# Kernel optimization log

Hardware: AMD Instinct MI355X
Metric: run time of the kernel (lower is better)

Reference implementation:

```python
import math
import jax, jax.numpy as jnp
import numpy as np

H, W = 24, 24
N = H * W
D = 1024
B = 32
MAX_ITERS = 6

# 9 relative neighbor offsets (3x3 window, row-major)
_REL = np.array([[-1, -1], [-1, 0], [-1, 1], [0, -1], [0, 0], [0, 1], [1, -1], [1, 0], [1, 1]])


def _neighbor_cols():
    y, x = np.meshgrid(np.arange(H), np.arange(W), indexing='ij')
    ny = np.clip(y[None] + _REL[:, 0, None, None], 0, H - 1)  # [9,H,W]
    nx = np.clip(x[None] + _REL[:, 1, None, None], 0, W - 1)
    return jnp.asarray((ny * W + nx).reshape(9, N))  # [9,N]


def setup_inputs() -> dict:
    key = jax.random.key(0)
    ks = jax.random.split(key, 8)
    return {
        'tok2d': jax.random.normal(ks[0], (B, N + 1, D), dtype=jnp.float32),
        'dw_w': jax.random.normal(ks[1], (D, 1, 3, 3), dtype=jnp.float32) * 0.02,
        'pw_w': jax.random.normal(ks[2], (9, D, 1, 1), dtype=jnp.float32) * 0.02,
        'pw_b': jnp.zeros((9,), dtype=jnp.float32),
        'q_w': jax.random.normal(ks[3], (D, D), dtype=jnp.float32) * 0.02,
        'q_b': jax.random.normal(ks[4], (D,), dtype=jnp.float32) * 0.02,
        'v_w': jax.random.normal(ks[5], (D, D), dtype=jnp.float32) * 0.02,
        'v_b': jax.random.normal(ks[6], (D,), dtype=jnp.float32) * 0.02,
        'K': 256,
        'MAX_TOKENS': 128,
    }


def _affinity_head(patch2d, dw_w, pw_w, pw_b):
    # patch2d: [B,H,W,D] -> Q: [B,H,W,9]
    x = jnp.transpose(patch2d, (0, 3, 1, 2))  # NCHW
    x = jax.lax.conv_general_dilated(
        x, dw_w, window_strides=(1, 1), padding='SAME',
        feature_group_count=D,
        dimension_numbers=('NCHW', 'OIHW', 'NCHW'))
    x = jnp.einsum('bdhw,od->bohw', x, pw_w[:, :, 0, 0]) + pw_b[None, :, None, None]
    return jax.nn.softmax(jnp.transpose(x, (0, 2, 3, 1)), axis=-1)


def _build_token_affinity(Q):
    # Q: [B,H,W,9] -> A: [B,N,N] via 9 shifted-neighbor scatters
    cols = _neighbor_cols()                                   # [9,N]
    rows = jnp.broadcast_to(jnp.arange(N)[None, :], (9, N))   # [9,N]
    vals = jnp.moveaxis(Q.reshape(-1, N, 9), -1, 1).reshape(-1, 9 * N)  # [B,9*N]
    A = jnp.zeros((Q.shape[0], N, N), dtype=Q.dtype)
    return A.at[:, rows.reshape(-1), cols.reshape(-1)].add(vals)


def _cluster_roots(A):
    roots = jnp.argmax(A, axis=-1)  # [B,N]
    for _ in range(MAX_ITERS):      # pointer jumping (idempotent once converged)
        roots = jnp.take_along_axis(roots, roots, axis=1)
    return roots


def _cluster_centers(E, roots, K):
    b = E.shape[0]
    bidx = jnp.arange(b)[:, None]
    centers_sum = jnp.zeros_like(E).at[bidx, roots].add(E)          # [B,N,D]
    counts = jnp.zeros(E.shape[:2], E.dtype).at[bidx, roots].add(1.0)  # [B,N]
    _, topk_idx = jax.lax.top_k(counts, K)
    ord_idx = jnp.sort(topk_idx, axis=1)
    cs = jnp.take_along_axis(centers_sum, ord_idx[:, :, None], axis=1)
    cnt = jnp.take_along_axis(counts, ord_idx, axis=1)
    C = cs / jnp.clip(cnt, 1.0, None)[:, :, None]
    return C, cnt


def reference(tok2d, dw_w, pw_w, pw_b, q_w, q_b, v_w, v_b, K, MAX_TOKENS):
    cls_tok = tok2d[:, :1, :]                 # [B,1,D]
    patch = tok2d[:, 1:, :]                   # [B,N,D]
    Q = _affinity_head(patch.reshape(-1, H, W, D), dw_w, pw_w, pw_b)
    A = _build_token_affinity(Q)
    roots = _cluster_roots(A)
    C, cnt = _cluster_centers(patch, roots, K)
    Q_cls = cls_tok @ q_w.T + q_b             # [B,1,D]
    K_v = C @ v_w.T + v_b                     # [B,K,D]
    scores = jnp.einsum('bod,bkd->bk', Q_cls, K_v) / math.sqrt(D)
    valid = jnp.where(cnt > 0, scores, -jnp.inf)
    m = min(MAX_TOKENS, C.shape[1])
    _, idx = jax.lax.top_k(valid, m)
    idx_sorted = jnp.sort(idx, axis=-1)
    return jnp.take_along_axis(C, idx_sorted[:, :, None], axis=1)  # [B,m,D]
```

## Files before the change

kernel.cpp:

```cpp
#include <hip/hip_runtime.h>
#include <math.h>

#define Hh 24
#define Ww 24
#define Nn 576
#define Dd 1024
#define Bb 32
#define Kk 256
#define Mm 128
#define TOKSTRIDE (577 * 1024)

#define R0_OFF 0
#define MEMB_OFF 1152
#define OFFS_OFF 1728
#define ORD_OFF 2304
#define CNT_OFF 2560
#define P_OFF 2944
#define QC_OFF 3776
#define U_OFF 4800
#define T_OFF 5824
#define UP_OFF 6144

__device__ __forceinline__ float* batch_base(float* out, int b) {
  return out + (size_t)b * Mm * Dd;
}

__device__ __forceinline__ float wave_sum_dpp(float x) {
  int y;
  y = __builtin_amdgcn_update_dpp(0, __float_as_int(x), 0x111, 0xf, 0xf, true);
  x += __int_as_float(y);
  y = __builtin_amdgcn_update_dpp(0, __float_as_int(x), 0x112, 0xf, 0xf, true);
  x += __int_as_float(y);
  y = __builtin_amdgcn_update_dpp(0, __float_as_int(x), 0x114, 0xf, 0xf, true);
  x += __int_as_float(y);
  y = __builtin_amdgcn_update_dpp(0, __float_as_int(x), 0x118, 0xf, 0xf, true);
  x += __int_as_float(y);
  y = __builtin_amdgcn_update_dpp(0, __float_as_int(x), 0x142, 0xa, 0xf, true);
  x += __int_as_float(y);
  y = __builtin_amdgcn_update_dpp(0, __float_as_int(x), 0x143, 0xc, 0xf, true);
  x += __int_as_float(y);
  return x;
}

__global__ __launch_bounds__(256) void qcls_kernel(
    const float* __restrict__ tok2d, const float* __restrict__ q_w,
    const float* __restrict__ q_b, float* __restrict__ outb) {
  int dp = blockIdx.x;
  int wave = threadIdx.x >> 6;
  int lane = threadIdx.x & 63;
  float4 qv[4];
#pragma unroll
  for (int i = 0; i < 4; i++)
    qv[i] = *(const float4*)(q_w + (size_t)dp * Dd + lane * 4 + 256 * i);
  float qb = q_b[dp];
  for (int bb = 0; bb < 8; bb++) {
    int b = wave * 8 + bb;
    const float* cls = tok2d + (size_t)b * TOKSTRIDE;
    float a = 0.f;
#pragma unroll
    for (int i = 0; i < 4; i++) {
      float4 cv = *(const float4*)(cls + lane * 4 + 256 * i);
      a += qv[i].x * cv.x + qv[i].y * cv.y + qv[i].z * cv.z + qv[i].w * cv.w;
    }
    a = wave_sum_dpp(a);
    if (lane == 63) batch_base(outb, b)[QC_OFF + dp] = a + qb;
  }
}

__global__ __launch_bounds__(256) void u_part_kernel(const float* __restrict__ v_w,
                                                     float* __restrict__ outb) {
  int b = blockIdx.x >> 3;
  int chunk = blockIdx.x & 7;
  int tid = threadIdx.x;
  int d0 = tid * 4;
  float* basef = batch_base(outb, b);
  __shared__ float qs[128];
  if (tid < 128) qs[tid] = basef[QC_OFF + chunk * 128 + tid];
  __syncthreads();
  float4 a = make_float4(0.f, 0.f, 0.f, 0.f);
#pragma unroll 4
  for (int dpl = 0; dpl < 128; dpl++) {
    int dp = chunk * 128 + dpl;
    float4 vv = *(const float4*)(v_w + (size_t)dp * Dd + d0);
    float qq = qs[dpl];
    a.x += qq * vv.x; a.y += qq * vv.y; a.z += qq * vv.z; a.w += qq * vv.w;
  }
  *(float4*)(basef + UP_OFF + chunk * Dd + d0) = a;
}

__global__ __launch_bounds__(256) void combine_ut_kernel(
    const float* __restrict__ v_b, float* __restrict__ outb) {
  int b = blockIdx.x;
  int tid = threadIdx.x;
  float* basef = batch_base(outb, b);
  int d0 = tid * 4;
  float4 s = make_float4(0.f, 0.f, 0.f, 0.f);
#pragma unroll
  for (int c = 0; c < 8; c++) {
    float4 v = *(const float4*)(basef + UP_OFF + c * Dd + d0);
    s.x += v.x; s.y += v.y; s.z += v.z; s.w += v.w;
  }
  *(float4*)(basef + U_OFF + d0) = s;

  float a = 0.f;
  for (int i = tid; i < Dd; i += 256) a += basef[QC_OFF + i] * v_b[i];
  __shared__ float sh[256];
  sh[tid] = a;
  __syncthreads();
  for (int st = 128; st > 0; st >>= 1) {
    if (tid < st) sh[tid] += sh[tid + st];
    __syncthreads();
  }
  if (tid == 0) basef[T_OFF] = sh[0];
}

__global__ __launch_bounds__(256, 3) void affinity_p_root_kernel(
    const float* __restrict__ tok2d, const float* __restrict__ dw_w,
    const float* __restrict__ pw_w, const float* __restrict__ pw_b,
    float* __restrict__ outb) {
  int wave = threadIdx.x >> 6;
  int lane = threadIdx.x & 63;
  int blk = (blockIdx.x & 7) * (Bb * Hh * 3 / 8) + (blockIdx.x >> 3);
  int b = blk / (Hh * 3);
  int rem = blk % (Hh * 3);
  int y = rem / 3;
  int x0 = (rem % 3) * 8;
  int d0 = wave * 256 + lane * 4;
  const float* patch = tok2d + (size_t)b * TOKSTRIDE + Dd;
  float* basef = batch_base(outb, b);

  union { float4 v[9]; float f[36]; } w;
  const float4* dwp = (const float4*)(dw_w + (size_t)d0 * 9);
#pragma unroll
  for (int j = 0; j < 9; j++) w.v[j] = dwp[j];
  float4 pw[9];
#pragma unroll
  for (int o = 0; o < 9; o++)
    pw[o] = *(const float4*)(pw_w + (size_t)o * Dd + d0);
  float4 u4 = *(const float4*)(basef + U_OFF + d0);

  __shared__ float red[8][4][10];

  float4 cc[8];
  float pacc[8];
#pragma unroll
  for (int t = 0; t < 8; t++) {
    cc[t] = make_float4(0.f, 0.f, 0.f, 0.f);
    pacc[t] = 0.f;
  }
#pragma unroll
  for (int ky = 0; ky < 3; ky++) {
    int yy = y + ky - 1;
    if (yy < 0 || yy >= Hh) continue;
    const float* prow = patch + (size_t)(yy * Ww) * Dd + d0;
    float4 wA = make_float4(0.f, 0.f, 0.f, 0.f);
    if (x0 > 0) wA = *(const float4*)(prow + (size_t)(x0 - 1) * Dd);
    float4 wB = *(const float4*)(prow + (size_t)x0 * Dd);
    int kA = ky * 3, kB = ky * 3 + 1, kC = ky * 3 + 2;
#pragma unroll
    for (int t = 0; t < 8; t++) {
      float4 wC = make_float4(0.f, 0.f, 0.f, 0.f);
      int xx = x0 + t + 1;
      if (xx < Ww) wC = *(const float4*)(prow + (size_t)xx * Dd);
      cc[t].x += wA.x * w.f[kA] + wB.x * w.f[kB] + wC.x * w.f[kC];
      cc[t].y += wA.y * w.f[9 + kA] + wB.y * w.f[9 + kB] + wC.y * w.f[9 + kC];
      cc[t].z += wA.z * w.f[18 + kA] + wB.z * w.f[18 + kB] + wC.z * w.f[18 + kC];
      cc[t].w += wA.w * w.f[27 + kA] + wB.w * w.f[27 + kB] + wC.w * w.f[27 + kC];
      if (ky == 1)
        pacc[t] = wB.x * u4.x + wB.y * u4.y + wB.z * u4.z + wB.w * u4.w;
      wA = wB;
      wB = wC;
    }
  }

#pragma unroll
  for (int t = 0; t < 8; t++) {
    float acc[10];
#pragma unroll
    for (int o = 0; o < 9; o++) {
      acc[o] = cc[t].x * pw[o].x + cc[t].y * pw[o].y + cc[t].z * pw[o].z +
               cc[t].w * pw[o].w;
    }
    acc[9] = pacc[t];
#pragma unroll
    for (int o = 0; o < 10; o++) acc[o] = wave_sum_dpp(acc[o]);
    if (lane == 63) {
#pragma unroll
      for (int o = 0; o < 10; o++) red[t][wave][o] = acc[o];
    }
  }
  __syncthreads();

  if (threadIdx.x < 8) {
    int t = threadIdx.x;
    int x = x0 + t;
    int n = y * Ww + x;
    float l[9], q[9];
    float mx = -INFINITY;
#pragma unroll
    for (int o = 0; o < 9; o++) {
      l[o] = red[t][0][o] + red[t][1][o] + red[t][2][o] + red[t][3][o] + pw_b[o];
      mx = fmaxf(mx, l[o]);
    }
    float ssum = 0.f;
#pragma unroll
    for (int o = 0; o < 9; o++) {
      q[o] = expf(l[o] - mx);
      ssum += q[o];
    }
#pragma unroll
    for (int o = 0; o < 9; o++) q[o] = q[o] / ssum;

    int cols[9];
    float vals[9];
    int ncol = 0;
    for (int o = 0; o < 9; o++) {
      int dy = o / 3 - 1, dx = o % 3 - 1;
      int ny = min(max(y + dy, 0), Hh - 1);
      int nx = min(max(x + dx, 0), Ww - 1);
      int col = ny * Ww + nx;
      int f = -1;
      for (int j = 0; j < ncol; j++)
        if (cols[j] == col) { f = j; break; }
      if (f >= 0) vals[f] += q[o];
      else { cols[ncol] = col; vals[ncol] = q[o]; ncol++; }
    }
    float best = -1.f;
    int bcol = 1 << 30;
    for (int j = 0; j < ncol; j++) {
      if (vals[j] > best || (vals[j] == best && cols[j] < bcol)) {
        best = vals[j];
        bcol = cols[j];
      }
    }
    ((int*)basef)[R0_OFF + n] = bcol;
    basef[P_OFF + n] = red[t][0][9] + red[t][1][9] + red[t][2][9] + red[t][3][9];
  }
}

__global__ __launch_bounds__(576) void cluster_topk_kernel(float* __restrict__ outb) {
  int b = blockIdx.x;
  int n = threadIdx.x;
  int* base = (int*)batch_base(outb, b);
  __shared__ int ra[Nn], rb[Nn], scnt[Nn], soff[Nn];
  ra[n] = base[R0_OFF + n];
  scnt[n] = 0;
  __syncthreads();
  for (int it = 0; it < 6; it++) {
    rb[n] = ra[ra[n]];
    __syncthreads();
    ra[n] = rb[n];
    __syncthreads();
  }
  int r = ra[n];
  atomicAdd(&scnt[r], 1);
  __syncthreads();

  soff[n] = scnt[n];
  __syncthreads();
  for (int s = 1; s < Nn; s <<= 1) {
    int v = (n >= s) ? soff[n - s] : 0;
    __syncthreads();
    soff[n] += v;
    __syncthreads();
  }
  int excl = soff[n] - scnt[n];
  base[OFFS_OFF + n] = excl;
  int offr = soff[r] - scnt[r];
  int rk = 0;
  for (int m = 0; m < n; m++) rk += (ra[m] == r);
  base[MEMB_OFF + offr + rk] = n;

  int cn = scnt[n];
  int rank = 0;
  for (int m = 0; m < Nn; m++) {
    int cm = scnt[m];
    rank += (cm > cn) || (cm == cn && m < n);
  }
  int sl = (rank < Kk) ? 1 : 0;
  rb[n] = sl;
  __syncthreads();
  for (int s = 1; s < Nn; s <<= 1) {
    int v = (n >= s) ? rb[n - s] : 0;
    __syncthreads();
    rb[n] += v;
    __syncthreads();
  }
  if (sl) {
    int pos = rb[n] - 1;
    base[ORD_OFF + pos] = n;
    base[CNT_OFF + pos] = cn;
  }
}

__global__ __launch_bounds__(256) void scores_plan_kernel(float* __restrict__ outb) {
  int b = blockIdx.x;
  int tid = threadIdx.x;
  int wave = tid >> 6, lane = tid & 63;
  float* basef = batch_base(outb, b);
  int* base = (int*)basef;
  __shared__ int s_mem[Nn], s_off[Nn], s_ord[Kk], s_cnt[Kk], s_out[Mm];
  __shared__ float ss[Kk];
  __shared__ int sel[Kk];
  for (int i = tid; i < Nn; i += 256) {
    s_mem[i] = base[MEMB_OFF + i];
    s_off[i] = base[OFFS_OFF + i];
  }
  s_ord[tid] = base[ORD_OFF + tid];
  s_cnt[tid] = base[CNT_OFF + tid];
  float tt = basef[T_OFF];
  __syncthreads();

  int idx = s_ord[tid];
  int c = s_cnt[tid];
  float s;
  if (c > 0) {
    int off = s_off[idx];
    float sum = 0.f;
    for (int j = 0; j < c; j++) sum += basef[P_OFF + s_mem[off + j]];
    s = (sum / (float)c + tt) * (1.0f / 32.0f);
  } else {
    s = -INFINITY;
  }
  ss[tid] = s;
  __syncthreads();

  float vk = ss[tid];
  int rank = 0;
  for (int m = 0; m < Kk; m++) {
    float vm = ss[m];
    rank += (vm > vk) || (vm == vk && m < tid);
  }
  sel[tid] = (rank < Mm) ? 1 : 0;
  __syncthreads();
  if (sel[tid]) {
    int pos = 0;
    for (int m = 0; m < tid; m++) pos += sel[m];
    s_out[pos] = tid;
  }
  __syncthreads();

  for (int kp = wave; kp < Mm; kp += 4) {
    int k = s_out[kp];
    int kidx = s_ord[k];
    int kc = s_cnt[k];
    int koff = s_off[kidx];
    int* row = base + kp * Dd;
    if (lane == 0) row[0] = kc;
    for (int j = lane; j < kc; j += 64) row[1 + j] = s_mem[koff + j];
  }
}

__global__ __launch_bounds__(256) void output_kernel(
    const float* __restrict__ tok2d, float* __restrict__ outb) {
  int blk = blockIdx.x;
  int b = blk / Mm;
  int tid = threadIdx.x;
  float* rowf = outb + (size_t)blk * Dd;
  int* rowi = (int*)rowf;
  __shared__ int s_c;
  __shared__ int s_m[Nn];
  if (tid == 0) s_c = rowi[0];
  __syncthreads();
  int c = s_c;
  for (int j = tid; j < c; j += 256) s_m[j] = rowi[1 + j];
  __syncthreads();
  const float* patch = tok2d + (size_t)b * TOKSTRIDE + Dd;
  int d0 = tid * 4;
  float4 acc = make_float4(0.f, 0.f, 0.f, 0.f);
  for (int j = 0; j < c; j++) {
    float4 rv = *(const float4*)(patch + (size_t)s_m[j] * Dd + d0);
    acc.x += rv.x; acc.y += rv.y; acc.z += rv.z; acc.w += rv.w;
  }
  float inv = 1.0f / (float)max(c, 1);
  *(float4*)(rowf + d0) =
      make_float4(acc.x * inv, acc.y * inv, acc.z * inv, acc.w * inv);
}

extern "C" void kernel_launch(void* const* d_in, const int* in_sizes, int n_in,
                              void* d_out, int out_size, void* d_ws,
                              size_t ws_size, hipStream_t stream) {
  const float* tok2d = (const float*)d_in[0];
  const float* dw_w = (const float*)d_in[1];
  const float* pw_w = (const float*)d_in[2];
  const float* pw_b = (const float*)d_in[3];
  const float* q_w = (const float*)d_in[4];
  const float* q_b = (const float*)d_in[5];
  const float* v_w = (const float*)d_in[6];
  const float* v_b = (const float*)d_in[7];
  float* out = (float*)d_out;
  (void)d_ws; (void)ws_size;

  qcls_kernel<<<dim3(Dd), dim3(256), 0, stream>>>(tok2d, q_w, q_b, out);
  u_part_kernel<<<dim3(Bb * 8), dim3(256), 0, stream>>>(v_w, out);
  combine_ut_kernel<<<dim3(Bb), dim3(256), 0, stream>>>(v_b, out);
  affinity_p_root_kernel<<<dim3(Bb * Hh * 3), dim3(256), 0, stream>>>(
      tok2d, dw_w, pw_w, pw_b, out);
  cluster_topk_kernel<<<dim3(Bb), dim3(Nn), 0, stream>>>(out);
  scores_plan_kernel<<<dim3(Bb), dim3(256), 0, stream>>>(out);
  output_kernel<<<dim3(Bb * Mm), dim3(256), 0, stream>>>(tok2d, out);
}
```

Before: 249.7 us.

## Raise affinity kernel occupancy, defer pw loads, shorten DPP reduction, unroll root selection

```diff
diff --git a/kernel.cpp b/kernel.cpp
--- a/kernel.cpp
+++ b/kernel.cpp
@@ -42,6 +42,19 @@
   return x;
 }
 
+__device__ __forceinline__ float row_sum_dpp(float x) {
+  int y;
+  y = __builtin_amdgcn_update_dpp(0, __float_as_int(x), 0x111, 0xf, 0xf, true);
+  x += __int_as_float(y);
+  y = __builtin_amdgcn_update_dpp(0, __float_as_int(x), 0x112, 0xf, 0xf, true);
+  x += __int_as_float(y);
+  y = __builtin_amdgcn_update_dpp(0, __float_as_int(x), 0x114, 0xf, 0xf, true);
+  x += __int_as_float(y);
+  y = __builtin_amdgcn_update_dpp(0, __float_as_int(x), 0x118, 0xf, 0xf, true);
+  x += __int_as_float(y);
+  return x;
+}
+
 __global__ __launch_bounds__(256) void qcls_kernel(
     const float* __restrict__ tok2d, const float* __restrict__ q_w,
     const float* __restrict__ q_b, float* __restrict__ outb) {
@@ -114,7 +127,7 @@
   if (tid == 0) basef[T_OFF] = sh[0];
 }
 
-__global__ __launch_bounds__(256, 3) void affinity_p_root_kernel(
+__global__ __launch_bounds__(256, 4) void affinity_p_root_kernel(
     const float* __restrict__ tok2d, const float* __restrict__ dw_w,
     const float* __restrict__ pw_w, const float* __restrict__ pw_b,
     float* __restrict__ outb) {
@@ -129,17 +142,13 @@
   const float* patch = tok2d + (size_t)b * TOKSTRIDE + Dd;
   float* basef = batch_base(outb, b);
 
+  __shared__ float red[8 * 167 + 8];
+
   union { float4 v[9]; float f[36]; } w;
   const float4* dwp = (const float4*)(dw_w + (size_t)d0 * 9);
 #pragma unroll
   for (int j = 0; j < 9; j++) w.v[j] = dwp[j];
-  float4 pw[9];
-#pragma unroll
-  for (int o = 0; o < 9; o++)
-    pw[o] = *(const float4*)(pw_w + (size_t)o * Dd + d0);
   float4 u4 = *(const float4*)(basef + U_OFF + d0);
-
-  __shared__ float red[8][4][10];
 
   float4 cc[8];
   float pacc[8];
@@ -173,6 +182,13 @@
     }
   }
 
+  __builtin_amdgcn_sched_barrier(0);
+
+  float4 pw[9];
+#pragma unroll
+  for (int o = 0; o < 9; o++)
+    pw[o] = *(const float4*)(pw_w + (size_t)o * Dd + d0);
+
 #pragma unroll
   for (int t = 0; t < 8; t++) {
     float acc[10];
@@ -183,23 +199,31 @@
     }
     acc[9] = pacc[t];
 #pragma unroll
-    for (int o = 0; o < 10; o++) acc[o] = wave_sum_dpp(acc[o]);
-    if (lane == 63) {
-#pragma unroll
-      for (int o = 0; o < 10; o++) red[t][wave][o] = acc[o];
-    }
-  }
-  __syncthreads();
-
-  if (threadIdx.x < 8) {
-    int t = threadIdx.x;
+    for (int o = 0; o < 10; o++) acc[o] = row_sum_dpp(acc[o]);
+    if ((lane & 15) == 15) {
+      int r = wave * 4 + (lane >> 4);
+#pragma unroll
+      for (int o = 0; o < 10; o++) red[t * 167 + r * 10 + o] = acc[o];
+    }
+  }
+  __syncthreads();
+
+  if (lane < 2) {
+    int t = wave * 2 + lane;
     int x = x0 + t;
     int n = y * Ww + x;
-    float l[9], q[9];
+    float l[10];
+#pragma unroll
+    for (int o = 0; o < 10; o++) l[o] = 0.f;
+    for (int r = 0; r < 16; r++) {
+#pragma unroll
+      for (int o = 0; o < 10; o++) l[o] += red[t * 167 + r * 10 + o];
+    }
+    float q[9];
     float mx = -INFINITY;
 #pragma unroll
     for (int o = 0; o < 9; o++) {
-      l[o] = red[t][0][o] + red[t][1][o] + red[t][2][o] + red[t][3][o] + pw_b[o];
+      l[o] += pw_b[o];
       mx = fmaxf(mx, l[o]);
     }
     float ssum = 0.f;
@@ -211,30 +235,29 @@
 #pragma unroll
     for (int o = 0; o < 9; o++) q[o] = q[o] / ssum;
 
-    int cols[9];
-    float vals[9];
-    int ncol = 0;
+    int colv[9];
+#pragma unroll
     for (int o = 0; o < 9; o++) {
       int dy = o / 3 - 1, dx = o % 3 - 1;
       int ny = min(max(y + dy, 0), Hh - 1);
       int nx = min(max(x + dx, 0), Ww - 1);
-      int col = ny * Ww + nx;
-      int f = -1;
-      for (int j = 0; j < ncol; j++)
-        if (cols[j] == col) { f = j; break; }
-      if (f >= 0) vals[f] += q[o];
-      else { cols[ncol] = col; vals[ncol] = q[o]; ncol++; }
+      colv[o] = ny * Ww + nx;
     }
     float best = -1.f;
     int bcol = 1 << 30;
-    for (int j = 0; j < ncol; j++) {
-      if (vals[j] > best || (vals[j] == best && cols[j] < bcol)) {
-        best = vals[j];
-        bcol = cols[j];
+#pragma unroll
+    for (int o = 0; o < 9; o++) {
+      float v = 0.f;
+#pragma unroll
+      for (int oo = 0; oo < 9; oo++)
+        v = (colv[oo] == colv[o]) ? v + q[oo] : v;
+      if (v > best || (v == best && colv[o] < bcol)) {
+        best = v;
+        bcol = colv[o];
       }
     }
     ((int*)basef)[R0_OFF + n] = bcol;
-    basef[P_OFF + n] = red[t][0][9] + red[t][1][9] + red[t][2][9] + red[t][3][9];
+    basef[P_OFF + n] = l[9];
   }
 }
 
```

Result: no change. 246.1 us (-1.4%).
